# Kernel optimization log

Hardware: AMD Instinct MI355X
Metric: run time of the kernel (lower is better)

The kernel has to match this reference:

```python
import jax, jax.numpy as jnp
import numpy as np

NUM_HEADS = 8
KEY_DIM = 64
WINDOW = 8
SHIFT = 4
B, H, W, C = 8, 64, 64, 512


def setup_inputs() -> dict:
    key = jax.random.key(0)
    ks = jax.random.split(key, 6)
    s = 0.02  # small init scale for numerically tame attention
    return {
        "x": jax.random.normal(ks[0], (B, H, W, C), jnp.float32),
        "wq": jax.random.normal(ks[1], (C, NUM_HEADS, KEY_DIM), jnp.float32) * s,
        "bq": jnp.zeros((NUM_HEADS, KEY_DIM), jnp.float32),
        "wk": jax.random.normal(ks[2], (C, NUM_HEADS, KEY_DIM), jnp.float32) * s,
        "bk": jnp.zeros((NUM_HEADS, KEY_DIM), jnp.float32),
        "wv": jax.random.normal(ks[3], (C, NUM_HEADS, KEY_DIM), jnp.float32) * s,
        "bv": jnp.zeros((NUM_HEADS, KEY_DIM), jnp.float32),
        "wo": jax.random.normal(ks[4], (NUM_HEADS, KEY_DIM, C), jnp.float32) * s,
        "bo": jnp.zeros((C,), jnp.float32),
    }


def reference(x, wq, bq, wk, bk, wv, bv, wo, bo):
    b, h, w, c = x.shape
    ws, ss = WINDOW, SHIFT
    pad_h = (ws - h % ws) % ws
    pad_w = (ws - w % ws) % ws
    padded = jnp.pad(x, ((0, 0), (0, pad_h), (0, pad_w), (0, 0)))
    if ss:
        padded = jnp.roll(padded, shift=(-ss, -ss), axis=(1, 2))
    ph, pw = h + pad_h, w + pad_w
    nh, nw = ph // ws, pw // ws
    # window partition: [B, nh, ws, nw, ws, C] -> [B*nh*nw, ws*ws, C]
    win = padded.reshape(b, nh, ws, nw, ws, c)
    win = win.transpose(0, 1, 3, 2, 4, 5).reshape(-1, ws * ws, c)
    q = jnp.einsum("ntc,chd->nthd", win, wq) + bq
    k = jnp.einsum("ntc,chd->nthd", win, wk) + bk
    v = jnp.einsum("ntc,chd->nthd", win, wv) + bv
    scale = 1.0 / jnp.sqrt(jnp.asarray(KEY_DIM, q.dtype))
    scores = jnp.einsum("nqhd,nkhd->nhqk", q, k) * scale
    attn = jax.nn.softmax(scores, axis=-1)
    out = jnp.einsum("nhqk,nkhd->nqhd", attn, v)
    proj = jnp.einsum("nqhd,hdc->nqc", out, wo) + bo
    # window merge
    merged = proj.reshape(b, nh, nw, ws, ws, c)
    merged = merged.transpose(0, 1, 3, 2, 4, 5).reshape(b, ph, pw, c)
    if ss:
        merged = jnp.roll(merged, shift=(ss, ss), axis=(1, 2))
    if pad_h or pad_w:
        merged = merged[:, :h, :w, :]
    return x + merged
```

## Files before the change

### kernel.cpp

```cpp
#include <hip/hip_runtime.h>

typedef unsigned short u16;
typedef short bf16x8 __attribute__((ext_vector_type(8)));
typedef float f32x4 __attribute__((ext_vector_type(4)));

typedef __attribute__((address_space(3))) unsigned int lds_uint;
typedef __attribute__((address_space(1))) const unsigned int glob_uint;

__device__ __forceinline__ void gll16(const void* g, void* l) {
    __builtin_amdgcn_global_load_lds((glob_uint*)g, (lds_uint*)l, 16, 0, 0);
}

__device__ __forceinline__ u16 f2b(float f) {
    union { float f; unsigned int u; } cv; cv.f = f;
    unsigned int u = cv.u;
    u += 0x7fffu + ((u >> 16) & 1u);
    return (u16)(u >> 16);
}

__global__ void prep_kernel(const float* __restrict__ wq, const float* __restrict__ wk,
                            const float* __restrict__ wv, const float* __restrict__ wo,
                            const float* __restrict__ bq, const float* __restrict__ bk,
                            const float* __restrict__ bv,
                            u16* __restrict__ wqkvT, u16* __restrict__ woT,
                            float* __restrict__ biasq) {
    int idx = blockIdx.x * 256 + threadIdx.x;
    const int N1 = 512 * 1536;
    const int N2 = 512 * 512;
    if (idx < N1) {
        int k = idx / 1536, n = idx % 1536;
        int which = n >> 9, nn = n & 511;
        const float* w = (which == 0) ? wq : (which == 1) ? wk : wv;
        wqkvT[n * 512 + k] = f2b(w[k * 512 + nn]);
    } else if (idx < N1 + N2) {
        int j = idx - N1;
        int k = j / 512, n = j % 512;
        woT[n * 512 + k] = f2b(wo[k * 512 + n]);
    } else if (idx < N1 + N2 + 1536) {
        int n = idx - N1 - N2;
        biasq[n] = (n < 512) ? bq[n] : (n < 1024) ? bk[n - 512] : bv[n - 1024];
    }
}

__global__ __launch_bounds__(256) void pre_kernel(const float* __restrict__ x,
                                                  u16* __restrict__ xw) {
    int idx = blockIdx.x * 256 + threadIdx.x;
    int row = idx >> 6;
    int c = (idx & 63) * 8;
    int b_ = row >> 12, win = (row >> 6) & 63, t = row & 63;
    int wi = win >> 3, wj = win & 7, ti = t >> 3, tj = t & 7;
    int hh = (wi * 8 + ti + 4) & 63, ww = (wj * 8 + tj + 4) & 63;
    const float* src = x + ((size_t)b_ * 4096 + hh * 64 + ww) * 512 + c;
    float4 v0 = *(const float4*)src;
    float4 v1 = *(const float4*)(src + 4);
    ushort4 p0, p1;
    p0.x = f2b(v0.x); p0.y = f2b(v0.y); p0.z = f2b(v0.z); p0.w = f2b(v0.w);
    p1.x = f2b(v1.x); p1.y = f2b(v1.y); p1.z = f2b(v1.z); p1.w = f2b(v1.w);
    u16* dst = xw + (size_t)row * 512 + c;
    *(ushort4*)dst = p0;
    *(ushort4*)(dst + 4) = p1;
}

__global__ __launch_bounds__(256) void qkv_gemm(const u16* __restrict__ xw,
        const u16* __restrict__ wqkvT, const float* __restrict__ biasq,
        u16* __restrict__ qws, u16* __restrict__ kws, u16* __restrict__ vws) {
    __shared__ u16 As[128 * 32];
    __shared__ u16 Bs[128 * 32];
    const int tid = threadIdx.x;
    const int lane = tid & 63, wid = tid >> 6;
    const int wr = wid >> 1, wc = wid & 1;
    const int m = lane & 15, qd = lane >> 4;
    const int rowBase = blockIdx.y * 128;
    const int colBase = blockIdx.x * 128;

    f32x4 acc[4][4];
#pragma unroll
    for (int i = 0; i < 4; ++i)
#pragma unroll
        for (int j = 0; j < 4; ++j) acc[i][j] = (f32x4){0.f, 0.f, 0.f, 0.f};

    for (int kt = 0; kt < 16; ++kt) {
        const int k0 = kt * 32;
        __syncthreads();
#pragma unroll
        for (int j = 0; j < 2; ++j) {
            int q = j * 256 + tid;
            int r = q >> 2;
            int cc = (q & 3) ^ (r & 3);
            gll16(xw + (size_t)(rowBase + r) * 512 + k0 + cc * 8, &As[q * 8]);
            gll16(wqkvT + (size_t)(colBase + r) * 512 + k0 + cc * 8, &Bs[q * 8]);
        }
        __syncthreads();
        bf16x8 a[4], b[4];
#pragma unroll
        for (int ni = 0; ni < 4; ++ni) {
            int R = wc * 64 + ni * 16 + m;
            b[ni] = *(const bf16x8*)&Bs[R * 32 + ((qd ^ (R & 3)) * 8)];
        }
#pragma unroll
        for (int mi = 0; mi < 4; ++mi) {
            int R = wr * 64 + mi * 16 + m;
            a[mi] = *(const bf16x8*)&As[R * 32 + ((qd ^ (R & 3)) * 8)];
        }
#pragma unroll
        for (int mi = 0; mi < 4; ++mi)
#pragma unroll
            for (int ni = 0; ni < 4; ++ni)
                acc[mi][ni] = __builtin_amdgcn_mfma_f32_16x16x32_bf16(a[mi], b[ni], acc[mi][ni], 0, 0, 0);
    }

    const int which = colBase >> 9;
    u16* dst = (which == 0) ? qws : (which == 1) ? kws : vws;
#pragma unroll
    for (int mi = 0; mi < 4; ++mi) {
#pragma unroll
        for (int rr = 0; rr < 4; ++rr) {
            int row = rowBase + wr * 64 + mi * 16 + qd * 4 + rr;
            int win = row >> 6, t = row & 63;
#pragma unroll
            for (int ni = 0; ni < 4; ++ni) {
                int col = colBase + wc * 64 + ni * 16 + m;
                float v = acc[mi][ni][rr] + biasq[col];
                int h = (col >> 6) & 7, d = col & 63;
                if (which < 2)
                    dst[((size_t)(win * 8 + h) * 64 + t) * 64 + d] = f2b(v);
                else
                    dst[((size_t)(win * 8 + h) * 64 + d) * 64 + t] = f2b(v);
            }
        }
    }
}

__global__ __launch_bounds__(256) void attn_kernel(const u16* __restrict__ qws,
        const u16* __restrict__ kws, const u16* __restrict__ vws,
        u16* __restrict__ ows) {
    __shared__ u16 P[4 * 64 * 72];
    const int tid = threadIdx.x, lane = tid & 63, wid = tid >> 6;
    const int task = blockIdx.x * 4 + wid;
    const int win = task >> 3, h = task & 7;
    const int m = lane & 15, qd = lane >> 4;
    const u16* Qp = qws + (size_t)(win * 8 + h) * 4096;
    const u16* Kp = kws + (size_t)(win * 8 + h) * 4096;
    const u16* Vp = vws + (size_t)(win * 8 + h) * 4096;

    bf16x8 qa[4][2], ka[4][2];
#pragma unroll
    for (int mi = 0; mi < 4; ++mi)
#pragma unroll
        for (int s = 0; s < 2; ++s) {
            qa[mi][s] = *(const bf16x8*)(Qp + (mi * 16 + m) * 64 + s * 32 + qd * 8);
            ka[mi][s] = *(const bf16x8*)(Kp + (mi * 16 + m) * 64 + s * 32 + qd * 8);
        }
    f32x4 sa[4][4];
#pragma unroll
    for (int i = 0; i < 4; ++i)
#pragma unroll
        for (int j = 0; j < 4; ++j) sa[i][j] = (f32x4){0.f, 0.f, 0.f, 0.f};
#pragma unroll
    for (int mi = 0; mi < 4; ++mi)
#pragma unroll
        for (int ni = 0; ni < 4; ++ni)
#pragma unroll
            for (int s = 0; s < 2; ++s)
                sa[mi][ni] = __builtin_amdgcn_mfma_f32_16x16x32_bf16(qa[mi][s], ka[ni][s], sa[mi][ni], 0, 0, 0);

    const float c1 = 0.125f * 1.4426950408889634f;
    u16* Pl = P + wid * 64 * 72;
#pragma unroll
    for (int mi = 0; mi < 4; ++mi) {
#pragma unroll
        for (int rr = 0; rr < 4; ++rr) {
            float mx = -3.4e38f;
#pragma unroll
            for (int ni = 0; ni < 4; ++ni) mx = fmaxf(mx, sa[mi][ni][rr]);
            mx = fmaxf(mx, __shfl_xor(mx, 1, 64));
            mx = fmaxf(mx, __shfl_xor(mx, 2, 64));
            mx = fmaxf(mx, __shfl_xor(mx, 4, 64));
            mx = fmaxf(mx, __shfl_xor(mx, 8, 64));
            float sum = 0.f;
#pragma unroll
            for (int ni = 0; ni < 4; ++ni) {
                float p = exp2f((sa[mi][ni][rr] - mx) * c1);
                sa[mi][ni][rr] = p;
                sum += p;
            }
            sum += __shfl_xor(sum, 1, 64);
            sum += __shfl_xor(sum, 2, 64);
            sum += __shfl_xor(sum, 4, 64);
            sum += __shfl_xor(sum, 8, 64);
            float inv = 1.f / sum;
            int row = mi * 16 + qd * 4 + rr;
#pragma unroll
            for (int ni = 0; ni < 4; ++ni)
                Pl[row * 72 + ni * 16 + m] = f2b(sa[mi][ni][rr] * inv);
        }
    }

    bf16x8 pa[4][2], va[4][2];
#pragma unroll
    for (int mi = 0; mi < 4; ++mi)
#pragma unroll
        for (int s = 0; s < 2; ++s)
            pa[mi][s] = *(const bf16x8*)&Pl[(mi * 16 + m) * 72 + s * 32 + qd * 8];
#pragma unroll
    for (int ni = 0; ni < 4; ++ni)
#pragma unroll
        for (int s = 0; s < 2; ++s)
            va[ni][s] = *(const bf16x8*)(Vp + (ni * 16 + m) * 64 + s * 32 + qd * 8);
    f32x4 oa[4][4];
#pragma unroll
    for (int i = 0; i < 4; ++i)
#pragma unroll
        for (int j = 0; j < 4; ++j) oa[i][j] = (f32x4){0.f, 0.f, 0.f, 0.f};
#pragma unroll
    for (int mi = 0; mi < 4; ++mi)
#pragma unroll
        for (int ni = 0; ni < 4; ++ni)
#pragma unroll
            for (int s = 0; s < 2; ++s)
                oa[mi][ni] = __builtin_amdgcn_mfma_f32_16x16x32_bf16(pa[mi][s], va[ni][s], oa[mi][ni], 0, 0, 0);
#pragma unroll
    for (int mi = 0; mi < 4; ++mi)
#pragma unroll
        for (int rr = 0; rr < 4; ++rr) {
            int t = mi * 16 + qd * 4 + rr;
            u16* dst = ows + (size_t)(win * 64 + t) * 512 + h * 64;
#pragma unroll
            for (int ni = 0; ni < 4; ++ni)
                dst[ni * 16 + m] = f2b(oa[mi][ni][rr]);
        }
}

__global__ __launch_bounds__(256) void proj_gemm(const u16* __restrict__ ows,
        const u16* __restrict__ woT, const float* __restrict__ bo,
        const float* __restrict__ x, float* __restrict__ out) {
    __shared__ u16 As[128 * 32];
    __shared__ u16 Bs[128 * 32];
    const int tid = threadIdx.x;
    const int lane = tid & 63, wid = tid >> 6;
    const int wr = wid >> 1, wc = wid & 1;
    const int m = lane & 15, qd = lane >> 4;
    const int rowBase = blockIdx.y * 128;
    const int colBase = blockIdx.x * 128;

    f32x4 acc[4][4];
#pragma unroll
    for (int i = 0; i < 4; ++i)
#pragma unroll
        for (int j = 0; j < 4; ++j) acc[i][j] = (f32x4){0.f, 0.f, 0.f, 0.f};

    for (int kt = 0; kt < 16; ++kt) {
        const int k0 = kt * 32;
        __syncthreads();
#pragma unroll
        for (int j = 0; j < 2; ++j) {
            int q = j * 256 + tid;
            int r = q >> 2;
            int cc = (q & 3) ^ (r & 3);
            gll16(ows + (size_t)(rowBase + r) * 512 + k0 + cc * 8, &As[q * 8]);
            gll16(woT + (size_t)(colBase + r) * 512 + k0 + cc * 8, &Bs[q * 8]);
        }
        __syncthreads();
        bf16x8 a[4], b[4];
#pragma unroll
        for (int ni = 0; ni < 4; ++ni) {
            int R = wc * 64 + ni * 16 + m;
            b[ni] = *(const bf16x8*)&Bs[R * 32 + ((qd ^ (R & 3)) * 8)];
        }
#pragma unroll
        for (int mi = 0; mi < 4; ++mi) {
            int R = wr * 64 + mi * 16 + m;
            a[mi] = *(const bf16x8*)&As[R * 32 + ((qd ^ (R & 3)) * 8)];
        }
#pragma unroll
        for (int mi = 0; mi < 4; ++mi)
#pragma unroll
            for (int ni = 0; ni < 4; ++ni)
                acc[mi][ni] = __builtin_amdgcn_mfma_f32_16x16x32_bf16(a[mi], b[ni], acc[mi][ni], 0, 0, 0);
    }

#pragma unroll
    for (int mi = 0; mi < 4; ++mi) {
#pragma unroll
        for (int rr = 0; rr < 4; ++rr) {
            int row = rowBase + wr * 64 + mi * 16 + qd * 4 + rr;
            int win = row >> 6, t = row & 63;
            int b_ = win >> 6, wh = (win >> 3) & 7, ww_ = win & 7;
            int ti = t >> 3, tj = t & 7;
            int hh = (wh * 8 + ti + 4) & 63;
            int www = (ww_ * 8 + tj + 4) & 63;
            size_t tok = (size_t)b_ * 4096 + hh * 64 + www;
#pragma unroll
            for (int ni = 0; ni < 4; ++ni) {
                int col = colBase + wc * 64 + ni * 16 + m;
                out[tok * 512 + col] = acc[mi][ni][rr] + bo[col] + x[tok * 512 + col];
            }
        }
    }
}

extern "C" void kernel_launch(void* const* d_in, const int* in_sizes, int n_in,
                              void* d_out, int out_size, void* d_ws, size_t ws_size,
                              hipStream_t stream) {
    const float* x  = (const float*)d_in[0];
    const float* wq = (const float*)d_in[1];
    const float* bq = (const float*)d_in[2];
    const float* wk = (const float*)d_in[3];
    const float* bk = (const float*)d_in[4];
    const float* wv = (const float*)d_in[5];
    const float* bv = (const float*)d_in[6];
    const float* wo = (const float*)d_in[7];
    const float* bo = (const float*)d_in[8];
    float* out = (float*)d_out;
    char* ws = (char*)d_ws;

    u16*   wqkvT = (u16*)ws;
    u16*   woT   = (u16*)(ws + 1572864);
    float* biasq = (float*)(ws + 1572864 + 524288);
    size_t off = 2103296;
    u16* xw  = (u16*)(ws + off);
    u16* qws = xw + (size_t)16777216;
    u16* kws = qws + (size_t)16777216;
    u16* vws = kws + (size_t)16777216;
    u16* ows = xw;

    const int prepN = 512 * 1536 + 512 * 512 + 1536;
    prep_kernel<<<dim3((prepN + 255) / 256), dim3(256), 0, stream>>>(
        wq, wk, wv, wo, bq, bk, bv, wqkvT, woT, biasq);
    pre_kernel<<<dim3(8192), dim3(256), 0, stream>>>(x, xw);
    qkv_gemm<<<dim3(12, 256), dim3(256), 0, stream>>>(xw, wqkvT, biasq, qws, kws, vws);
    attn_kernel<<<dim3(1024), dim3(256), 0, stream>>>(qws, kws, vws, ows);
    proj_gemm<<<dim3(4, 256), dim3(256), 0, stream>>>(ows, woT, bo, x, out);
}
```

Before: 311.2 us.

## Store QKV row-major, transpose V in LDS, and double GEMM K-tile

The QKV GEMM now writes one row-major [token, 1536] bf16 buffer instead of scattering into per-head Q/K/V layouts, where V was stored transposed with strided 2-byte writes. The attention kernel reads Q, K and V straight from that buffer and transposes V through LDS before the PV MFMA. Both GEMMs use a 64-wide K tile with an 8-way XOR swizzle, which halves the number of barrier-separated iterations. The costs are more LDS per block, which may lower occupancy, and scalar LDS gathers for the V transpose.

```diff
diff --git a/kernel.cpp b/kernel.cpp
--- a/kernel.cpp
+++ b/kernel.cpp
@@ -63,15 +63,16 @@
 
 __global__ __launch_bounds__(256) void qkv_gemm(const u16* __restrict__ xw,
         const u16* __restrict__ wqkvT, const float* __restrict__ biasq,
-        u16* __restrict__ qws, u16* __restrict__ kws, u16* __restrict__ vws) {
-    __shared__ u16 As[128 * 32];
-    __shared__ u16 Bs[128 * 32];
+        u16* __restrict__ qkvb) {
+    __shared__ u16 As[128 * 64];
+    __shared__ u16 Bs[128 * 64];
     const int tid = threadIdx.x;
     const int lane = tid & 63, wid = tid >> 6;
     const int wr = wid >> 1, wc = wid & 1;
     const int m = lane & 15, qd = lane >> 4;
     const int rowBase = blockIdx.y * 128;
     const int colBase = blockIdx.x * 128;
+    const int c8 = (lane & 7) ^ (lane >> 3);
 
     f32x4 acc[4][4];
 #pragma unroll
@@ -79,78 +80,80 @@
 #pragma unroll
         for (int j = 0; j < 4; ++j) acc[i][j] = (f32x4){0.f, 0.f, 0.f, 0.f};
 
-    for (int kt = 0; kt < 16; ++kt) {
-        const int k0 = kt * 32;
+    for (int kt = 0; kt < 8; ++kt) {
+        const int k0 = kt * 64;
         __syncthreads();
 #pragma unroll
-        for (int j = 0; j < 2; ++j) {
-            int q = j * 256 + tid;
-            int r = q >> 2;
-            int cc = (q & 3) ^ (r & 3);
-            gll16(xw + (size_t)(rowBase + r) * 512 + k0 + cc * 8, &As[q * 8]);
-            gll16(wqkvT + (size_t)(colBase + r) * 512 + k0 + cc * 8, &Bs[q * 8]);
+        for (int j = 0; j < 4; ++j) {
+            int q = (j * 4 + wid) * 64 + lane;
+            int r = (j * 4 + wid) * 8 + (lane >> 3);
+            gll16(xw + (size_t)(rowBase + r) * 512 + k0 + c8 * 8, &As[q * 8]);
+            gll16(wqkvT + (size_t)(colBase + r) * 512 + k0 + c8 * 8, &Bs[q * 8]);
         }
         __syncthreads();
-        bf16x8 a[4], b[4];
-#pragma unroll
-        for (int ni = 0; ni < 4; ++ni) {
-            int R = wc * 64 + ni * 16 + m;
-            b[ni] = *(const bf16x8*)&Bs[R * 32 + ((qd ^ (R & 3)) * 8)];
-        }
-#pragma unroll
-        for (int mi = 0; mi < 4; ++mi) {
-            int R = wr * 64 + mi * 16 + m;
-            a[mi] = *(const bf16x8*)&As[R * 32 + ((qd ^ (R & 3)) * 8)];
-        }
-#pragma unroll
-        for (int mi = 0; mi < 4; ++mi)
-#pragma unroll
-            for (int ni = 0; ni < 4; ++ni)
-                acc[mi][ni] = __builtin_amdgcn_mfma_f32_16x16x32_bf16(a[mi], b[ni], acc[mi][ni], 0, 0, 0);
-    }
-
-    const int which = colBase >> 9;
-    u16* dst = (which == 0) ? qws : (which == 1) ? kws : vws;
+#pragma unroll
+        for (int s = 0; s < 2; ++s) {
+            bf16x8 a[4], b[4];
+#pragma unroll
+            for (int ni = 0; ni < 4; ++ni) {
+                int R = wc * 64 + ni * 16 + m;
+                b[ni] = *(const bf16x8*)&Bs[R * 64 + (((s * 4 + qd) ^ (R & 7)) * 8)];
+            }
+#pragma unroll
+            for (int mi = 0; mi < 4; ++mi) {
+                int R = wr * 64 + mi * 16 + m;
+                a[mi] = *(const bf16x8*)&As[R * 64 + (((s * 4 + qd) ^ (R & 7)) * 8)];
+            }
+#pragma unroll
+            for (int mi = 0; mi < 4; ++mi)
+#pragma unroll
+                for (int ni = 0; ni < 4; ++ni)
+                    acc[mi][ni] = __builtin_amdgcn_mfma_f32_16x16x32_bf16(a[mi], b[ni], acc[mi][ni], 0, 0, 0);
+        }
+    }
+
+    float bias[4];
+#pragma unroll
+    for (int ni = 0; ni < 4; ++ni) bias[ni] = biasq[colBase + wc * 64 + ni * 16 + m];
 #pragma unroll
     for (int mi = 0; mi < 4; ++mi) {
 #pragma unroll
         for (int rr = 0; rr < 4; ++rr) {
             int row = rowBase + wr * 64 + mi * 16 + qd * 4 + rr;
-            int win = row >> 6, t = row & 63;
-#pragma unroll
-            for (int ni = 0; ni < 4; ++ni) {
-                int col = colBase + wc * 64 + ni * 16 + m;
-                float v = acc[mi][ni][rr] + biasq[col];
-                int h = (col >> 6) & 7, d = col & 63;
-                if (which < 2)
-                    dst[((size_t)(win * 8 + h) * 64 + t) * 64 + d] = f2b(v);
-                else
-                    dst[((size_t)(win * 8 + h) * 64 + d) * 64 + t] = f2b(v);
-            }
-        }
-    }
-}
-
-__global__ __launch_bounds__(256) void attn_kernel(const u16* __restrict__ qws,
-        const u16* __restrict__ kws, const u16* __restrict__ vws,
-        u16* __restrict__ ows) {
-    __shared__ u16 P[4 * 64 * 72];
+            u16* dst = qkvb + (size_t)row * 1536 + colBase + wc * 64;
+#pragma unroll
+            for (int ni = 0; ni < 4; ++ni)
+                dst[ni * 16 + m] = f2b(acc[mi][ni][rr] + bias[ni]);
+        }
+    }
+}
+
+__global__ __launch_bounds__(256) void attn_kernel(const u16* __restrict__ qkvb,
+                                                   u16* __restrict__ ows) {
+    __shared__ u16 Sb[4 * 64 * 72];
     const int tid = threadIdx.x, lane = tid & 63, wid = tid >> 6;
     const int task = blockIdx.x * 4 + wid;
     const int win = task >> 3, h = task & 7;
     const int m = lane & 15, qd = lane >> 4;
-    const u16* Qp = qws + (size_t)(win * 8 + h) * 4096;
-    const u16* Kp = kws + (size_t)(win * 8 + h) * 4096;
-    const u16* Vp = vws + (size_t)(win * 8 + h) * 4096;
+    const u16* base = qkvb + (size_t)win * 64 * 1536;
+    u16* Sl = Sb + wid * 64 * 72;
 
     bf16x8 qa[4][2], ka[4][2];
 #pragma unroll
     for (int mi = 0; mi < 4; ++mi)
 #pragma unroll
         for (int s = 0; s < 2; ++s) {
-            qa[mi][s] = *(const bf16x8*)(Qp + (mi * 16 + m) * 64 + s * 32 + qd * 8);
-            ka[mi][s] = *(const bf16x8*)(Kp + (mi * 16 + m) * 64 + s * 32 + qd * 8);
-        }
+            const u16* p = base + (size_t)(mi * 16 + m) * 1536 + h * 64 + s * 32 + qd * 8;
+            qa[mi][s] = *(const bf16x8*)p;
+            ka[mi][s] = *(const bf16x8*)(p + 512);
+        }
+    bf16x8 vr[8];
+#pragma unroll
+    for (int i = 0; i < 8; ++i) {
+        int r = i * 8 + (lane >> 3);
+        vr[i] = *(const bf16x8*)(base + (size_t)r * 1536 + 1024 + h * 64 + (lane & 7) * 8);
+    }
+
     f32x4 sa[4][4];
 #pragma unroll
     for (int i = 0; i < 4; ++i)
@@ -165,7 +168,6 @@
                 sa[mi][ni] = __builtin_amdgcn_mfma_f32_16x16x32_bf16(qa[mi][s], ka[ni][s], sa[mi][ni], 0, 0, 0);
 
     const float c1 = 0.125f * 1.4426950408889634f;
-    u16* Pl = P + wid * 64 * 72;
 #pragma unroll
     for (int mi = 0; mi < 4; ++mi) {
 #pragma unroll
@@ -192,33 +194,40 @@
             int row = mi * 16 + qd * 4 + rr;
 #pragma unroll
             for (int ni = 0; ni < 4; ++ni)
-                Pl[row * 72 + ni * 16 + m] = f2b(sa[mi][ni][rr] * inv);
-        }
-    }
-
-    bf16x8 pa[4][2], va[4][2];
+                Sl[row * 72 + ni * 16 + m] = f2b(sa[mi][ni][rr] * inv);
+        }
+    }
+
+    bf16x8 pa[4][2];
 #pragma unroll
     for (int mi = 0; mi < 4; ++mi)
 #pragma unroll
         for (int s = 0; s < 2; ++s)
-            pa[mi][s] = *(const bf16x8*)&Pl[(mi * 16 + m) * 72 + s * 32 + qd * 8];
+            pa[mi][s] = *(const bf16x8*)&Sl[(mi * 16 + m) * 72 + s * 32 + qd * 8];
+
+#pragma unroll
+    for (int i = 0; i < 8; ++i) {
+        int r = i * 8 + (lane >> 3);
+        *(bf16x8*)&Sl[r * 72 + (lane & 7) * 8] = vr[i];
+    }
+    f32x4 oa[4][4];
+#pragma unroll
+    for (int i = 0; i < 4; ++i)
+#pragma unroll
+        for (int j = 0; j < 4; ++j) oa[i][j] = (f32x4){0.f, 0.f, 0.f, 0.f};
 #pragma unroll
     for (int ni = 0; ni < 4; ++ni)
 #pragma unroll
-        for (int s = 0; s < 2; ++s)
-            va[ni][s] = *(const bf16x8*)(Vp + (ni * 16 + m) * 64 + s * 32 + qd * 8);
-    f32x4 oa[4][4];
-#pragma unroll
-    for (int i = 0; i < 4; ++i)
-#pragma unroll
-        for (int j = 0; j < 4; ++j) oa[i][j] = (f32x4){0.f, 0.f, 0.f, 0.f};
-#pragma unroll
-    for (int mi = 0; mi < 4; ++mi)
-#pragma unroll
-        for (int ni = 0; ni < 4; ++ni)
-#pragma unroll
-            for (int s = 0; s < 2; ++s)
-                oa[mi][ni] = __builtin_amdgcn_mfma_f32_16x16x32_bf16(pa[mi][s], va[ni][s], oa[mi][ni], 0, 0, 0);
+        for (int s = 0; s < 2; ++s) {
+            bf16x8 v;
+#pragma unroll
+            for (int j = 0; j < 8; ++j)
+                ((short*)&v)[j] = (short)Sl[(s * 32 + qd * 8 + j) * 72 + ni * 16 + m];
+#pragma unroll
+            for (int mi = 0; mi < 4; ++mi)
+                oa[mi][ni] = __builtin_amdgcn_mfma_f32_16x16x32_bf16(pa[mi][s], v, oa[mi][ni], 0, 0, 0);
+        }
+
 #pragma unroll
     for (int mi = 0; mi < 4; ++mi)
 #pragma unroll
@@ -234,14 +243,15 @@
 __global__ __launch_bounds__(256) void proj_gemm(const u16* __restrict__ ows,
         const u16* __restrict__ woT, const float* __restrict__ bo,
         const float* __restrict__ x, float* __restrict__ out) {
-    __shared__ u16 As[128 * 32];
-    __shared__ u16 Bs[128 * 32];
+    __shared__ u16 As[128 * 64];
+    __shared__ u16 Bs[128 * 64];
     const int tid = threadIdx.x;
     const int lane = tid & 63, wid = tid >> 6;
     const int wr = wid >> 1, wc = wid & 1;
     const int m = lane & 15, qd = lane >> 4;
     const int rowBase = blockIdx.y * 128;
     const int colBase = blockIdx.x * 128;
+    const int c8 = (lane & 7) ^ (lane >> 3);
 
     f32x4 acc[4][4];
 #pragma unroll
@@ -249,34 +259,36 @@
 #pragma unroll
         for (int j = 0; j < 4; ++j) acc[i][j] = (f32x4){0.f, 0.f, 0.f, 0.f};
 
-    for (int kt = 0; kt < 16; ++kt) {
-        const int k0 = kt * 32;
+    for (int kt = 0; kt < 8; ++kt) {
+        const int k0 = kt * 64;
         __syncthreads();
 #pragma unroll
-        for (int j = 0; j < 2; ++j) {
-            int q = j * 256 + tid;
-            int r = q >> 2;
-            int cc = (q & 3) ^ (r & 3);
-            gll16(ows + (size_t)(rowBase + r) * 512 + k0 + cc * 8, &As[q * 8]);
-            gll16(woT + (size_t)(colBase + r) * 512 + k0 + cc * 8, &Bs[q * 8]);
+        for (int j = 0; j < 4; ++j) {
+            int q = (j * 4 + wid) * 64 + lane;
+            int r = (j * 4 + wid) * 8 + (lane >> 3);
+            gll16(ows + (size_t)(rowBase + r) * 512 + k0 + c8 * 8, &As[q * 8]);
+            gll16(woT + (size_t)(colBase + r) * 512 + k0 + c8 * 8, &Bs[q * 8]);
         }
         __syncthreads();
-        bf16x8 a[4], b[4];
-#pragma unroll
-        for (int ni = 0; ni < 4; ++ni) {
-            int R = wc * 64 + ni * 16 + m;
-            b[ni] = *(const bf16x8*)&Bs[R * 32 + ((qd ^ (R & 3)) * 8)];
-        }
-#pragma unroll
-        for (int mi = 0; mi < 4; ++mi) {
-            int R = wr * 64 + mi * 16 + m;
-            a[mi] = *(const bf16x8*)&As[R * 32 + ((qd ^ (R & 3)) * 8)];
-        }
-#pragma unroll
-        for (int mi = 0; mi < 4; ++mi)
-#pragma unroll
-            for (int ni = 0; ni < 4; ++ni)
-                acc[mi][ni] = __builtin_amdgcn_mfma_f32_16x16x32_bf16(a[mi], b[ni], acc[mi][ni], 0, 0, 0);
+#pragma unroll
+        for (int s = 0; s < 2; ++s) {
+            bf16x8 a[4], b[4];
+#pragma unroll
+            for (int ni = 0; ni < 4; ++ni) {
+                int R = wc * 64 + ni * 16 + m;
+                b[ni] = *(const bf16x8*)&Bs[R * 64 + (((s * 4 + qd) ^ (R & 7)) * 8)];
+            }
+#pragma unroll
+            for (int mi = 0; mi < 4; ++mi) {
+                int R = wr * 64 + mi * 16 + m;
+                a[mi] = *(const bf16x8*)&As[R * 64 + (((s * 4 + qd) ^ (R & 7)) * 8)];
+            }
+#pragma unroll
+            for (int mi = 0; mi < 4; ++mi)
+#pragma unroll
+                for (int ni = 0; ni < 4; ++ni)
+                    acc[mi][ni] = __builtin_amdgcn_mfma_f32_16x16x32_bf16(a[mi], b[ni], acc[mi][ni], 0, 0, 0);
+        }
     }
 
 #pragma unroll
@@ -318,17 +330,15 @@
     u16*   woT   = (u16*)(ws + 1572864);
     float* biasq = (float*)(ws + 1572864 + 524288);
     size_t off = 2103296;
-    u16* xw  = (u16*)(ws + off);
-    u16* qws = xw + (size_t)16777216;
-    u16* kws = qws + (size_t)16777216;
-    u16* vws = kws + (size_t)16777216;
-    u16* ows = xw;
+    u16* xw   = (u16*)(ws + off);
+    u16* qkvb = xw + (size_t)16777216;
+    u16* ows  = xw;
 
     const int prepN = 512 * 1536 + 512 * 512 + 1536;
     prep_kernel<<<dim3((prepN + 255) / 256), dim3(256), 0, stream>>>(
         wq, wk, wv, wo, bq, bk, bv, wqkvT, woT, biasq);
     pre_kernel<<<dim3(8192), dim3(256), 0, stream>>>(x, xw);
-    qkv_gemm<<<dim3(12, 256), dim3(256), 0, stream>>>(xw, wqkvT, biasq, qws, kws, vws);
-    attn_kernel<<<dim3(1024), dim3(256), 0, stream>>>(qws, kws, vws, ows);
+    qkv_gemm<<<dim3(12, 256), dim3(256), 0, stream>>>(xw, wqkvT, biasq, qkvb);
+    attn_kernel<<<dim3(1024), dim3(256), 0, stream>>>(qkvb, ows);
     proj_gemm<<<dim3(4, 256), dim3(256), 0, stream>>>(ows, woT, bo, x, out);
 }
```

New measurement: 278.3 us. -10.6%, faster.
